# Kernel optimization log

Measured on AMD Instinct MI355X. Metric: run time of the kernel, lower is better.

Reference implementation:

```python
import jax, jax.numpy as jnp
import numpy as np

EMBED_DIM = 768
NUM_HEADS = 12
HEAD_DIM = EMBED_DIM // NUM_HEADS


def setup_inputs() -> dict:
    key = jax.random.key(0)
    ks = jax.random.split(key, 9)
    s = 1.0 / np.sqrt(EMBED_DIM)
    inp = {
        "x": jax.random.normal(ks[0], (4, 2048, EMBED_DIM), dtype=jnp.float32),
        "W_q": jax.random.uniform(ks[1], (EMBED_DIM, EMBED_DIM), jnp.float32, -s, s),
        "b_q": jax.random.uniform(ks[2], (EMBED_DIM,), jnp.float32, -s, s),
        "W_k": jax.random.uniform(ks[3], (EMBED_DIM, EMBED_DIM), jnp.float32, -s, s),
        "b_k": jax.random.uniform(ks[4], (EMBED_DIM,), jnp.float32, -s, s),
        "W_v": jax.random.uniform(ks[5], (EMBED_DIM, EMBED_DIM), jnp.float32, -s, s),
        "b_v": jax.random.uniform(ks[6], (EMBED_DIM,), jnp.float32, -s, s),
        "W_out": jax.random.uniform(ks[7], (EMBED_DIM, EMBED_DIM), jnp.float32, -s, s),
        "b_out": jax.random.uniform(ks[8], (EMBED_DIM,), jnp.float32, -s, s),
    }
    return inp


def reference(x, W_q, b_q, W_k, b_k, W_v, b_v, W_out, b_out):
    B, N, D = x.shape
    H, Hd = NUM_HEADS, HEAD_DIM
    scale = 1.0 / jnp.sqrt(jnp.asarray(Hd, x.dtype))
    # QKV projections (torch Linear: x @ W.T + b)
    Q = (x @ W_q.T + b_q).reshape(B, N, H, Hd).transpose(0, 2, 1, 3)  # (B,H,N,Hd)
    K = (x @ W_k.T + b_k).reshape(B, N, H, Hd).transpose(0, 2, 1, 3)
    V = (x @ W_v.T + b_v).reshape(B, N, H, Hd).transpose(0, 2, 1, 3)
    scores = jnp.einsum("bhqd,bhkd->bhqk", Q, K) * scale  # (B,H,N,N)
    attn = jax.nn.softmax(scores, axis=-1)
    out = jnp.einsum("bhqk,bhkd->bhqd", attn, V)  # (B,H,N,Hd)
    out = out.transpose(0, 2, 1, 3).reshape(B, N, D)
    return out @ W_out.T + b_out
```

## Files before the change

### kernel.cpp

```cpp
#include <hip/hip_runtime.h>
#include <math.h>

#define D_EMB 768
#define SEQN 2048
#define NB 4
#define NH 12
#define HDIM 64
#define MTOT (NB*SEQN)
#define SCLQ 0.18033688011112042f

typedef unsigned int u32;
typedef unsigned short u16;
typedef short sh4 __attribute__((ext_vector_type(4)));
typedef short bf16x8 __attribute__((ext_vector_type(8)));
typedef float f32x16 __attribute__((ext_vector_type(16)));

#define MFMA32(a,b,c) __builtin_amdgcn_mfma_f32_32x32x16_bf16((a),(b),(c),0,0,0)

__device__ __forceinline__ u32 cvtpk(float a, float b){
    u32 r; asm("v_cvt_pk_bf16_f32 %0, %1, %2" : "=v"(r) : "v"(a), "v"(b)); return r;
}
__device__ __forceinline__ u32 pack_split(float v){
    u32 h = cvtpk(v, v);
    float hf = __builtin_bit_cast(float, h << 16);
    float r = v - hf;
    u32 l = cvtpk(r, r);
    return __builtin_amdgcn_perm(l, h, 0x05040100u);
}
__device__ __forceinline__ void unpack4(uint4 p, sh4& hi, sh4& lo){
    u32 h0 = __builtin_amdgcn_perm(p.y, p.x, 0x05040100u);
    u32 h1 = __builtin_amdgcn_perm(p.w, p.z, 0x05040100u);
    u32 l0 = __builtin_amdgcn_perm(p.y, p.x, 0x07060302u);
    u32 l1 = __builtin_amdgcn_perm(p.w, p.z, 0x07060302u);
    uint2 h = {h0, h1}, l = {l0, l1};
    hi = __builtin_bit_cast(sh4, h);
    lo = __builtin_bit_cast(sh4, l);
}
__device__ __forceinline__ bf16x8 ldfrag(const short* p){
    sh4 a = *(const sh4*)p;
    sh4 b = *(const sh4*)(p+4);
    return __builtin_shufflevector(a,b,0,1,2,3,4,5,6,7);
}

__global__ __launch_bounds__(256) void pack_bf(const float* __restrict__ s, u16* __restrict__ d, int n4){
    int i = blockIdx.x*256 + threadIdx.x;
    if (i >= n4) return;
    float4 v = ((const float4*)s)[i];
    uint2 o = { cvtpk(v.x, v.y), cvtpk(v.z, v.w) };
    ((uint2*)d)[i] = o;
}
__global__ __launch_bounds__(256) void pack_wbf(const float* __restrict__ w0, const float* __restrict__ w1,
                                                const float* __restrict__ w2, const float* __restrict__ w3,
                                                u16* __restrict__ d, int n4){
    const int z = blockIdx.y;
    const float* s = (z==0)?w0:(z==1)?w1:(z==2)?w2:w3;
    int i = blockIdx.x*256 + threadIdx.x;
    if (i >= n4) return;
    float4 v = ((const float4*)s)[i];
    uint2 o = { cvtpk(v.x, v.y), cvtpk(v.z, v.w) };
    ((uint2*)(d + (size_t)z*n4*4))[i] = o;
}

#define GPAD 36

__global__ __launch_bounds__(256,3) void gemm_qkv(const u16* __restrict__ X, const u16* __restrict__ Wb,
        const float* __restrict__ bq, const float* __restrict__ bk, const float* __restrict__ bv,
        u16* __restrict__ oq, u16* __restrict__ okk, u16* __restrict__ ov){
    __shared__ __align__(16) short Ahi[128][GPAD];
    __shared__ __align__(16) short Bhi[128][GPAD];

    const int tid = threadIdx.x;
    const int l = tid & 63, w = tid >> 6;
    const int lq = l & 31, g = l >> 5;
    const int wm = w >> 1, wn = w & 1;
    const int m0 = blockIdx.x * 128;
    const int n0 = blockIdx.y * 128;
    const int z  = blockIdx.z;
    const u16* W = Wb + (size_t)z * D_EMB * D_EMB;
    const float* bias = (z==0) ? bq : (z==1) ? bk : bv;
    u16* out = (z==0) ? oq : (z==1) ? okk : ov;

    f32x16 acc[2][2];
    #pragma unroll
    for (int i=0;i<2;i++)
        #pragma unroll
        for (int j=0;j<2;j++)
            #pragma unroll
            for (int r=0;r<16;r++) acc[i][j][r] = 0.f;

    const int srow = tid >> 1;
    const int skb  = (tid & 1) * 16;
    const u16* ap0 = X + (size_t)(m0+srow)*D_EMB + skb;
    const u16* wp0 = W + (size_t)(n0+srow)*D_EMB + skb;

    uint4 a0 = *(const uint4*)ap0, a1 = *(const uint4*)(ap0+8);
    uint4 w0 = *(const uint4*)wp0, w1 = *(const uint4*)(wp0+8);

    for (int k0 = 0; k0 < D_EMB; k0 += 32) {
        __syncthreads();
        {
            uint2 t;
            t.x=a0.x; t.y=a0.y; *(uint2*)&Ahi[srow][skb]    = t;
            t.x=a0.z; t.y=a0.w; *(uint2*)&Ahi[srow][skb+4]  = t;
            t.x=a1.x; t.y=a1.y; *(uint2*)&Ahi[srow][skb+8]  = t;
            t.x=a1.z; t.y=a1.w; *(uint2*)&Ahi[srow][skb+12] = t;
            t.x=w0.x; t.y=w0.y; *(uint2*)&Bhi[srow][skb]    = t;
            t.x=w0.z; t.y=w0.w; *(uint2*)&Bhi[srow][skb+4]  = t;
            t.x=w1.x; t.y=w1.y; *(uint2*)&Bhi[srow][skb+8]  = t;
            t.x=w1.z; t.y=w1.w; *(uint2*)&Bhi[srow][skb+12] = t;
        }
        if (k0 + 32 < D_EMB){
            const u16* ap = ap0 + k0 + 32;
            const u16* wp = wp0 + k0 + 32;
            a0 = *(const uint4*)ap; a1 = *(const uint4*)(ap+8);
            w0 = *(const uint4*)wp; w1 = *(const uint4*)(wp+8);
        }
        __syncthreads();
        #pragma unroll
        for (int kk=0;kk<2;kk++){
            const int kc = kk*16 + g*8;
            bf16x8 ah[2], bh[2];
            #pragma unroll
            for (int i=0;i<2;i++) ah[i] = ldfrag(&Ahi[wm*64+32*i+lq][kc]);
            #pragma unroll
            for (int j=0;j<2;j++) bh[j] = ldfrag(&Bhi[wn*64+32*j+lq][kc]);
            #pragma unroll
            for (int i=0;i<2;i++)
                #pragma unroll
                for (int j=0;j<2;j++)
                    acc[i][j] = MFMA32(ah[i], bh[j], acc[i][j]);
        }
    }

    #pragma unroll
    for (int j=0;j<2;j++){
        const int c = n0 + wn*64 + 32*j + lq;
        const float bv2 = bias[c];
        #pragma unroll
        for (int i=0;i<2;i++){
            #pragma unroll
            for (int r=0;r<16;r++){
                const int m = m0 + wm*64 + 32*i + (r&3) + 8*(r>>2) + 4*g;
                float v = acc[i][j][r] + bv2;
                if (z==0) v *= SCLQ;
                const int b = m >> 11, n = m & 2047, h = c >> 6, hd = c & 63;
                out[(((size_t)(b*NH + h))*SEQN + n)*HDIM + hd] = (u16)cvtpk(v, v);
            }
        }
    }
}

__global__ __launch_bounds__(256,3) void gemm_out(const u32* __restrict__ A, const u16* __restrict__ Wb,
        const float* __restrict__ bo, float* __restrict__ outp){
    __shared__ __align__(16) short Ahi[128][GPAD];
    __shared__ __align__(16) short Alo[128][GPAD];
    __shared__ __align__(16) short Bhi[128][GPAD];

    const int tid = threadIdx.x;
    const int l = tid & 63, w = tid >> 6;
    const int lq = l & 31, g = l >> 5;
    const int wm = w >> 1, wn = w & 1;
    const int m0 = blockIdx.x * 128;
    const int n0 = blockIdx.y * 128;
    const u16* W = Wb + (size_t)3 * D_EMB * D_EMB;

    f32x16 acc[2][2];
    #pragma unroll
    for (int i=0;i<2;i++)
        #pragma unroll
        for (int j=0;j<2;j++)
            #pragma unroll
            for (int r=0;r<16;r++) acc[i][j][r] = 0.f;

    const int srow = tid >> 1;
    const int skb  = (tid & 1) * 16;
    const u32* ap0 = A + (size_t)(m0+srow)*D_EMB + skb;
    const u16* wp0 = W + (size_t)(n0+srow)*D_EMB + skb;

    uint4 areg[4];
    uint4 w0 = *(const uint4*)wp0, w1 = *(const uint4*)(wp0+8);
    #pragma unroll
    for (int c=0;c<4;c++) areg[c] = *(const uint4*)(ap0 + 4*c);

    for (int k0 = 0; k0 < D_EMB; k0 += 32) {
        __syncthreads();
        #pragma unroll
        for (int c=0;c<4;c++){
            sh4 h, lo2; unpack4(areg[c], h, lo2);
            *(sh4*)&Ahi[srow][skb+4*c] = h;
            *(sh4*)&Alo[srow][skb+4*c] = lo2;
        }
        {
            uint2 t;
            t.x=w0.x; t.y=w0.y; *(uint2*)&Bhi[srow][skb]    = t;
            t.x=w0.z; t.y=w0.w; *(uint2*)&Bhi[srow][skb+4]  = t;
            t.x=w1.x; t.y=w1.y; *(uint2*)&Bhi[srow][skb+8]  = t;
            t.x=w1.z; t.y=w1.w; *(uint2*)&Bhi[srow][skb+12] = t;
        }
        if (k0 + 32 < D_EMB){
            const u32* ap = ap0 + k0 + 32;
            const u16* wp = wp0 + k0 + 32;
            #pragma unroll
            for (int c=0;c<4;c++) areg[c] = *(const uint4*)(ap + 4*c);
            w0 = *(const uint4*)wp; w1 = *(const uint4*)(wp+8);
        }
        __syncthreads();
        #pragma unroll
        for (int kk=0;kk<2;kk++){
            const int kc = kk*16 + g*8;
            bf16x8 ah[2], al[2], bh[2];
            #pragma unroll
            for (int i=0;i<2;i++){
                ah[i] = ldfrag(&Ahi[wm*64+32*i+lq][kc]);
                al[i] = ldfrag(&Alo[wm*64+32*i+lq][kc]);
            }
            #pragma unroll
            for (int j=0;j<2;j++) bh[j] = ldfrag(&Bhi[wn*64+32*j+lq][kc]);
            #pragma unroll
            for (int i=0;i<2;i++)
                #pragma unroll
                for (int j=0;j<2;j++){
                    acc[i][j] = MFMA32(ah[i], bh[j], acc[i][j]);
                    acc[i][j] = MFMA32(al[i], bh[j], acc[i][j]);
                }
        }
    }

    #pragma unroll
    for (int j=0;j<2;j++){
        const int c = n0 + wn*64 + 32*j + lq;
        const float bv2 = bo[c];
        #pragma unroll
        for (int i=0;i<2;i++){
            #pragma unroll
            for (int r=0;r<16;r++){
                const int m = m0 + wm*64 + 32*i + (r&3) + 8*(r>>2) + 4*g;
                outp[(size_t)m*D_EMB + c] = acc[i][j][r] + bv2;
            }
        }
    }
}

#define KB 64
#define KPAD 68
#define NT (SEQN/KB)

__global__ __launch_bounds__(256,3) void attn_bf(const u16* __restrict__ Qg,
                                                 const u16* __restrict__ Kg,
                                                 const u16* __restrict__ Vg,
                                                 u32* __restrict__ Og) {
    __shared__ __align__(16) short Khi[2][KB][KPAD];
    __shared__ __align__(16) short Vthi[2][HDIM][KPAD];

    const int tid = threadIdx.x;
    const int l = tid & 63, w = tid >> 6;
    const int lq = l & 31, g = l >> 5;
    const int qt = blockIdx.x;
    const int bh = blockIdx.y;
    const size_t base = (size_t)bh * SEQN * HDIM;
    const int qrow = qt*128 + w*32 + lq;

    const int key = tid >> 2, dblk = (tid & 3) * 16;
    const int hd = tid & 63, kg = tid >> 6;
    const u16* kp0 = Kg + base + (size_t)key*HDIM + dblk;
    const u16* vp0 = Vg + base + (size_t)(kg*16)*HDIM + hd;

    bf16x8 qh[4];
    {
        const u16* qp = Qg + base + (size_t)qrow*HDIM;
        #pragma unroll
        for (int kk=0;kk<4;kk++){
            uint4 a = *(const uint4*)(qp + kk*16 + g*8);
            qh[kk] = __builtin_bit_cast(bf16x8, a);
        }
    }

    f32x16 o0, o1, zro;
    #pragma unroll
    for (int r=0;r<16;r++){ o0[r]=0.f; o1[r]=0.f; zro[r]=0.f; }
    float2 lr2 = {0.f, 0.f};

    uint4 kra, krb;
    u32 vt[16];

    auto loadTile = [&](int t){
        const u16* kp = kp0 + (size_t)t*KB*HDIM;
        const u16* vp = vp0 + (size_t)t*KB*HDIM;
        kra = *(const uint4*)kp;
        krb = *(const uint4*)(kp+8);
        #pragma unroll
        for (int i2=0;i2<16;i2++) vt[i2] = vp[(size_t)i2*HDIM];
    };
    auto stageWrite = [&](int cb){
        uint2 t;
        t.x=kra.x; t.y=kra.y; *(uint2*)&Khi[cb][key][dblk]    = t;
        t.x=kra.z; t.y=kra.w; *(uint2*)&Khi[cb][key][dblk+4]  = t;
        t.x=krb.x; t.y=krb.y; *(uint2*)&Khi[cb][key][dblk+8]  = t;
        t.x=krb.z; t.y=krb.w; *(uint2*)&Khi[cb][key][dblk+12] = t;
        #pragma unroll
        for (int c=0;c<4;c++){
            uint2 v2;
            v2.x = __builtin_amdgcn_perm(vt[4*c+1], vt[4*c+0], 0x05040100u);
            v2.y = __builtin_amdgcn_perm(vt[4*c+3], vt[4*c+2], 0x05040100u);
            *(uint2*)&Vthi[cb][hd][kg*16+4*c] = v2;
        }
    };

    loadTile(0);
    stageWrite(0);
    loadTile(1);

    for (int kt=0; kt<NT; kt++){
        const int cb = kt & 1;
        __syncthreads();
        if (kt+1 < NT){
            stageWrite(cb^1);
            if (kt+2 < NT) loadTile(kt+2);
        }

        f32x16 s0, s1;
        __builtin_amdgcn_s_setprio(1);
        {
            bf16x8 a0h = ldfrag(&Khi[cb][lq][0 + g*8]);
            bf16x8 a1h = ldfrag(&Khi[cb][32+lq][0 + g*8]);
            s0 = MFMA32(a0h, qh[0], zro);
            s1 = MFMA32(a1h, qh[0], zro);
        }
        #pragma unroll
        for (int kk=1;kk<4;kk++){
            const int kc = kk*16 + g*8;
            bf16x8 a0h = ldfrag(&Khi[cb][lq][kc]);
            bf16x8 a1h = ldfrag(&Khi[cb][32+lq][kc]);
            s0 = MFMA32(a0h, qh[kk], s0);
            s1 = MFMA32(a1h, qh[kk], s1);
        }
        __builtin_amdgcn_s_setprio(0);

        #pragma unroll
        for (int r=0;r<16;r++) s0[r] = __builtin_amdgcn_exp2f(s0[r]);
        #pragma unroll
        for (int r=0;r<16;r++) s1[r] = __builtin_amdgcn_exp2f(s1[r]);
        #pragma unroll
        for (int r=0;r<16;r+=2){
            float2 a = {s0[r], s0[r+1]};
            float2 b = {s1[r], s1[r+1]};
            lr2 += a;
            lr2 += b;
        }

        u32 pk0h[8], pk1h[8], rk0h[8], rk1h[8];
        #pragma unroll
        for (int j=0;j<8;j++){
            pk0h[j] = cvtpk(s0[2*j], s0[2*j+1]);
            pk1h[j] = cvtpk(s1[2*j], s1[2*j+1]);
        }
        #pragma unroll
        for (int j=0;j<8;j++){
            rk0h[j] = (u32)__shfl_xor((int)pk0h[j], 32);
            rk1h[j] = (u32)__shfl_xor((int)pk1h[j], 32);
        }

        u32 n0[2][4], n1[2][4];
        #pragma unroll
        for (int a2=0;a2<2;a2++){
            #pragma unroll
            for (int c=0;c<2;c++){
                n0[0][2*a2+c] = g ? rk0h[4*a2+2+c] : pk0h[4*a2+c];
                n1[0][2*a2+c] = g ? pk0h[4*a2+2+c] : rk0h[4*a2+c];
                n0[1][2*a2+c] = g ? rk1h[4*a2+2+c] : pk1h[4*a2+c];
                n1[1][2*a2+c] = g ? pk1h[4*a2+2+c] : rk1h[4*a2+c];
            }
        }

        __builtin_amdgcn_s_setprio(1);
        #pragma unroll
        for (int kk=0;kk<4;kk++){
            const int hblk = kk>>1, a2 = kk&1;
            uint4 whv = { n0[hblk][2*a2], n0[hblk][2*a2+1], n1[hblk][2*a2], n1[hblk][2*a2+1] };
            bf16x8 pbh = __builtin_bit_cast(bf16x8, whv);
            const int kc = kk*16 + g*8;
            bf16x8 v0h = ldfrag(&Vthi[cb][lq][kc]);
            bf16x8 v1h = ldfrag(&Vthi[cb][32+lq][kc]);
            o0 = MFMA32(v0h, pbh, o0);
            o1 = MFMA32(v1h, pbh, o1);
        }
        __builtin_amdgcn_s_setprio(0);
    }

    float l_run = lr2.x + lr2.y;
    l_run += __shfl_xor(l_run, 32);
    const float inv = 1.f / l_run;
    const int b = bh / NH, h = bh % NH;
    u32* op = Og + ((size_t)(b*SEQN + qrow))*D_EMB + h*HDIM;
    #pragma unroll
    for (int rq=0; rq<4; rq++){
        uint4 w0, w1;
        w0.x = pack_split(o0[4*rq+0]*inv); w0.y = pack_split(o0[4*rq+1]*inv);
        w0.z = pack_split(o0[4*rq+2]*inv); w0.w = pack_split(o0[4*rq+3]*inv);
        w1.x = pack_split(o1[4*rq+0]*inv); w1.y = pack_split(o1[4*rq+1]*inv);
        w1.z = pack_split(o1[4*rq+2]*inv); w1.w = pack_split(o1[4*rq+3]*inv);
        *(uint4*)(op + 8*rq + 4*g)      = w0;
        *(uint4*)(op + 32 + 8*rq + 4*g) = w1;
    }
}

extern "C" void kernel_launch(void* const* d_in, const int* in_sizes, int n_in,
                              void* d_out, int out_size, void* d_ws, size_t ws_size,
                              hipStream_t stream) {
    const float* x  = (const float*)d_in[0];
    const float* Wq = (const float*)d_in[1];
    const float* bq = (const float*)d_in[2];
    const float* Wk = (const float*)d_in[3];
    const float* bk = (const float*)d_in[4];
    const float* Wv = (const float*)d_in[5];
    const float* bv = (const float*)d_in[6];
    const float* Wo = (const float*)d_in[7];
    const float* bo = (const float*)d_in[8];

    const size_t per = (size_t)NB*NH*SEQN*HDIM;
    const size_t wplane = (size_t)D_EMB*D_EMB;
    u16* base16 = (u16*)d_ws;
    u16* Xbf = base16;
    u16* Qb  = base16 + per;
    u16* Kb  = base16 + 2*per;
    u16* Vb  = base16 + 3*per;
    u16* Wbf = base16 + 4*per;
    u32* ATpk = (u32*)(base16 + 4*per + 4*wplane);

    pack_bf<<<dim3((int)(per/4/256)), dim3(256), 0, stream>>>(x, Xbf, (int)(per/4));
    pack_wbf<<<dim3(576,4), dim3(256), 0, stream>>>(Wq, Wk, Wv, Wo, Wbf, (int)(wplane/4));

    gemm_qkv<<<dim3(MTOT/128, D_EMB/128, 3), dim3(256), 0, stream>>>(Xbf, Wbf, bq, bk, bv, Qb, Kb, Vb);

    attn_bf<<<dim3(SEQN/128, NB*NH), dim3(256), 0, stream>>>(Qb, Kb, Vb, ATpk);

    gemm_out<<<dim3(MTOT/128, D_EMB/128), dim3(256), 0, stream>>>(ATpk, Wbf, bo, (float*)d_out);
}
```

Before: 162.5 us.

## Software-pipeline QK^T of next tile with softmax/PV of current tile

Restructures the attention inner loop into a two-stage software pipeline: the QK MFMAs for tile t+1 are issued alongside the exp/pack/PV work of tile t, using two score register sets and a manually unrolled loop over tile pairs. The aim is to hide exp and shuffle latency behind matrix-core work. In exchange it doubles the barriers per tile and raises register pressure from the extra score accumulators. It also hardcodes the loop count at 15 pairs, which assumes NT=32.

```diff
diff --git a/kernel.cpp b/kernel.cpp
--- a/kernel.cpp
+++ b/kernel.cpp
@@ -305,24 +305,10 @@
             *(uint2*)&Vthi[cb][hd][kg*16+4*c] = v2;
         }
     };
-
-    loadTile(0);
-    stageWrite(0);
-    loadTile(1);
-
-    for (int kt=0; kt<NT; kt++){
-        const int cb = kt & 1;
-        __syncthreads();
-        if (kt+1 < NT){
-            stageWrite(cb^1);
-            if (kt+2 < NT) loadTile(kt+2);
-        }
-
-        f32x16 s0, s1;
-        __builtin_amdgcn_s_setprio(1);
+    auto qk = [&](int cb, f32x16& s0, f32x16& s1){
         {
-            bf16x8 a0h = ldfrag(&Khi[cb][lq][0 + g*8]);
-            bf16x8 a1h = ldfrag(&Khi[cb][32+lq][0 + g*8]);
+            bf16x8 a0h = ldfrag(&Khi[cb][lq][g*8]);
+            bf16x8 a1h = ldfrag(&Khi[cb][32+lq][g*8]);
             s0 = MFMA32(a0h, qh[0], zro);
             s1 = MFMA32(a1h, qh[0], zro);
         }
@@ -334,8 +320,8 @@
             s0 = MFMA32(a0h, qh[kk], s0);
             s1 = MFMA32(a1h, qh[kk], s1);
         }
-        __builtin_amdgcn_s_setprio(0);
-
+    };
+    auto finish = [&](int vb, f32x16& s0, f32x16& s1){
         #pragma unroll
         for (int r=0;r<16;r++) s0[r] = __builtin_amdgcn_exp2f(s0[r]);
         #pragma unroll
@@ -347,7 +333,6 @@
             lr2 += a;
             lr2 += b;
         }
-
         u32 pk0h[8], pk1h[8], rk0h[8], rk1h[8];
         #pragma unroll
         for (int j=0;j<8;j++){
@@ -359,7 +344,6 @@
             rk0h[j] = (u32)__shfl_xor((int)pk0h[j], 32);
             rk1h[j] = (u32)__shfl_xor((int)pk1h[j], 32);
         }
-
         u32 n0[2][4], n1[2][4];
         #pragma unroll
         for (int a2=0;a2<2;a2++){
@@ -371,21 +355,54 @@
                 n1[1][2*a2+c] = g ? pk1h[4*a2+2+c] : rk1h[4*a2+c];
             }
         }
-
-        __builtin_amdgcn_s_setprio(1);
         #pragma unroll
         for (int kk=0;kk<4;kk++){
             const int hblk = kk>>1, a2 = kk&1;
             uint4 whv = { n0[hblk][2*a2], n0[hblk][2*a2+1], n1[hblk][2*a2], n1[hblk][2*a2+1] };
             bf16x8 pbh = __builtin_bit_cast(bf16x8, whv);
             const int kc = kk*16 + g*8;
-            bf16x8 v0h = ldfrag(&Vthi[cb][lq][kc]);
-            bf16x8 v1h = ldfrag(&Vthi[cb][32+lq][kc]);
+            bf16x8 v0h = ldfrag(&Vthi[vb][lq][kc]);
+            bf16x8 v1h = ldfrag(&Vthi[vb][32+lq][kc]);
             o0 = MFMA32(v0h, pbh, o0);
             o1 = MFMA32(v1h, pbh, o1);
         }
+    };
+
+    f32x16 sA0, sA1, sB0, sB1;
+
+    loadTile(0);
+    stageWrite(0);
+    loadTile(1);
+    __syncthreads();
+    qk(0, sA0, sA1);
+
+    for (int p = 0; p < 15; p++){
+        const int t2 = 2*p + 2;
+        __syncthreads();
+        stageWrite(1);
+        loadTile(t2);
+        __syncthreads();
+        __builtin_amdgcn_s_setprio(1);
+        qk(1, sB0, sB1);
+        finish(0, sA0, sA1);
         __builtin_amdgcn_s_setprio(0);
-    }
+        __syncthreads();
+        stageWrite(0);
+        if (t2+1 < NT) loadTile(t2+1);
+        __syncthreads();
+        __builtin_amdgcn_s_setprio(1);
+        qk(0, sA0, sA1);
+        finish(1, sB0, sB1);
+        __builtin_amdgcn_s_setprio(0);
+    }
+    __syncthreads();
+    stageWrite(1);
+    __syncthreads();
+    __builtin_amdgcn_s_setprio(1);
+    qk(1, sB0, sB1);
+    finish(0, sA0, sA1);
+    finish(1, sB0, sB1);
+    __builtin_amdgcn_s_setprio(0);
 
     float l_run = lr2.x + lr2.y;
     l_run += __shfl_xor(l_run, 32);
```

After: 163.9 us. Within noise of the previous version (+0.8%).
